# Performance work log

Measured on AMD Instinct MI355X. Metric: run time of the kernel, lower is better.

Reference implementation:

```python
import jax, jax.numpy as jnp
import numpy as np

B, S, E = 2, 2048, 1024
D_ATTN, H = 1024, 16
HD = D_ATTN // H
SCALE = 1.0 / np.sqrt(D_ATTN)
ROPE_BASE = 10000.0


def setup_inputs() -> dict:
    key = jax.random.key(0)
    ks = jax.random.split(key, 7)
    def w(k, shape, scale):
        return jax.random.normal(k, shape, dtype=jnp.float32) * scale
    return {
        "q": w(ks[0], (B, S, E), 1.0),
        "k": w(ks[1], (B, S, E), 1.0),
        "v": w(ks[2], (B, S, E), 1.0),
        "Wq": w(ks[3], (D_ATTN, E), E ** -0.5),
        "Wk": w(ks[4], (D_ATTN, E), E ** -0.5),
        "Wv": w(ks[5], (D_ATTN, E), E ** -0.5),
        "Wo": w(ks[6], (E, D_ATTN), D_ATTN ** -0.5),
    }


def _rope(x):
    # x: [B, H, S, HD]; interleaved-pair rotary embedding over the seq axis
    s, d = x.shape[2], x.shape[3]
    half = d // 2
    inv_freq = 1.0 / (ROPE_BASE ** (jnp.arange(half, dtype=jnp.float32) * 2.0 / d))
    ang = jnp.arange(s, dtype=jnp.float32)[:, None] * inv_freq[None, :]  # [S, half]
    cos, sin = jnp.cos(ang), jnp.sin(ang)
    xr = x.reshape(x.shape[:-1] + (half, 2))
    x0, x1 = xr[..., 0], xr[..., 1]
    o0 = x0 * cos - x1 * sin
    o1 = x0 * sin + x1 * cos
    return jnp.stack([o0, o1], axis=-1).reshape(x.shape)


def reference(q, k, v, Wq, Wk, Wv, Wo):
    # linear projections (nn.Linear with weight [out, in]): y = x @ W^T
    qh = (q @ Wq.T).reshape(B, S, H, HD).transpose(0, 2, 1, 3)  # [B,H,S,HD]
    kh = (k @ Wk.T).reshape(B, S, H, HD).transpose(0, 2, 1, 3)
    vh = (v @ Wv.T).reshape(B, S, H, HD).transpose(0, 2, 1, 3)
    qh = _rope(qh)
    kh = _rope(kh)
    # shifted-causal mask: disallow j >= i (diagonal masked), except (0,0) allowed
    i = jnp.arange(S)[:, None]
    j = jnp.arange(S)[None, :]
    masked = j >= i                              # triu incl. diagonal
    masked = masked.at[0, 0].set(False)          # keep (0,0) so row 0 isn't all -inf
    scores = jnp.einsum("bhsd,bhtd->bhst", qh, kh) * SCALE
    scores = jnp.where(masked, -jnp.inf, scores)
    probs = jax.nn.softmax(scores, axis=-1)      # dropout omitted (eval mode)
    ctx = jnp.einsum("bhst,bhtd->bhsd", probs, vh)
    ctx = ctx.transpose(0, 2, 1, 3).reshape(B, S, D_ATTN)
    return ctx @ Wo.T
```

## Files before the change

kernel.cpp:

```cpp
#include <hip/hip_runtime.h>
#include <hip/hip_bf16.h>

#define BATCH 2
#define SEQ   2048
#define EMB   1024
#define DATTN 1024
#define NH    16
#define HD    64
#define MM    (BATCH*SEQ)
#define SCALE 0.03125f
#define MINIT -1.0e30f
#define ROPE_COEF 0.41524101186f

using bf16x8 = __attribute__((ext_vector_type(8))) short;
using f32x4  = __attribute__((ext_vector_type(4))) float;

__device__ inline short f2bf(float x) {
    __hip_bfloat16 b = __float2bfloat16(x);
    return *reinterpret_cast<short*>(&b);
}

__device__ inline void gl_lds16(const short* g, short* l) {
    __builtin_amdgcn_global_load_lds(
        (const __attribute__((address_space(1))) unsigned int*)g,
        (__attribute__((address_space(3))) unsigned int*)l, 16, 0, 0);
}

__global__ __launch_bounds__(256)
void cvt_all(const float* __restrict__ q, const float* __restrict__ k,
             const float* __restrict__ v,
             const float* __restrict__ Wq, const float* __restrict__ Wk,
             const float* __restrict__ Wv, const float* __restrict__ Wo,
             short* __restrict__ dst)
{
    const long QKV = (long)MM * EMB;
    const long WSZ = (long)DATTN * EMB;
    const long i = ((long)blockIdx.x * 256 + threadIdx.x) * 4;
    const float* s;
    long off;
    if (i < 3 * QKV) {
        const int seg = (int)(i / QKV);
        off = i - (long)seg * QKV;
        s = (seg == 0) ? q : (seg == 1) ? k : v;
    } else {
        const long j = i - 3 * QKV;
        const int seg = (int)(j / WSZ);
        off = j - (long)seg * WSZ;
        s = (seg == 0) ? Wq : (seg == 1) ? Wk : (seg == 2) ? Wv : Wo;
    }
    float4 x = *(const float4*)(s + off);
    short4 y;
    y.x = f2bf(x.x); y.y = f2bf(x.y); y.z = f2bf(x.z); y.w = f2bf(x.w);
    *(short4*)(dst + i) = y;
}

__device__ inline void stage_tile(const short* g, short* lds, int wave, int lane) {
    #pragma unroll
    for (int qq = 0; qq < 2; ++qq) {
        const int r = wave * 32 + qq * 16 + (lane >> 2);
        gl_lds16(g + (long)r * EMB + (lane & 3) * 8, lds + (wave * 2 + qq) * 512);
    }
}

__global__ __launch_bounds__(256)
void gemm_proj_bf16(const short* __restrict__ qb, const short* __restrict__ kb,
                    const short* __restrict__ vb,
                    const short* __restrict__ wqb, const short* __restrict__ wkb,
                    const short* __restrict__ wvb,
                    short* __restrict__ Qb, short* __restrict__ Kb,
                    short* __restrict__ Vtb)
{
    const short* A; const short* B;
    if (blockIdx.z == 0)      { A = qb; B = wqb; }
    else if (blockIdx.z == 1) { A = kb; B = wkb; }
    else                      { A = vb; B = wvb; }

    __shared__ short sA[128 * 32];
    __shared__ short sB[128 * 32];

    const int tid  = threadIdx.x;
    const int wave = tid >> 6, lane = tid & 63;
    const int quad = lane >> 4, l16 = lane & 15;
    const int wm = (wave >> 1) * 64, wn = (wave & 1) * 64;
    const long m0 = (long)blockIdx.x * 128, n0 = (long)blockIdx.y * 128;

    f32x4 acc[4][4];
    #pragma unroll
    for (int i = 0; i < 4; ++i)
        #pragma unroll
        for (int j = 0; j < 4; ++j) acc[i][j] = (f32x4){0.f, 0.f, 0.f, 0.f};

    for (int kt = 0; kt < EMB; kt += 32) {
        __syncthreads();
        stage_tile(A + m0 * EMB + kt, sA, wave, lane);
        stage_tile(B + n0 * EMB + kt, sB, wave, lane);
        __syncthreads();

        bf16x8 af[4], bfr[4];
        #pragma unroll
        for (int rt = 0; rt < 4; ++rt)
            af[rt] = *(const bf16x8*)&sA[(wm + rt * 16 + l16) * 32 + quad * 8];
        #pragma unroll
        for (int ct = 0; ct < 4; ++ct)
            bfr[ct] = *(const bf16x8*)&sB[(wn + ct * 16 + l16) * 32 + quad * 8];
        #pragma unroll
        for (int rt = 0; rt < 4; ++rt)
            #pragma unroll
            for (int ct = 0; ct < 4; ++ct)
                acc[rt][ct] = __builtin_amdgcn_mfma_f32_16x16x32_bf16(
                    af[rt], bfr[ct], acc[rt][ct], 0, 0, 0);
    }

    if (blockIdx.z < 2) {
        short* C = (blockIdx.z == 0) ? Qb : Kb;
        const float scl = (blockIdx.z == 0) ? SCALE : 1.0f;
        const int odd = l16 & 1;
        #pragma unroll
        for (int ct = 0; ct < 4; ++ct) {
            const long col = n0 + wn + ct * 16 + l16;
            const int hh = (int)(col >> 6), dd = (int)(col & (HD - 1));
            const float invf = exp2f(-ROPE_COEF * (float)(dd >> 1));
            #pragma unroll
            for (int rt = 0; rt < 4; ++rt) {
                #pragma unroll
                for (int reg = 0; reg < 4; ++reg) {
                    const long row = m0 + wm + rt * 16 + quad * 4 + reg;
                    const int bb = (int)(row >> 11), ss = (int)(row & (SEQ - 1));
                    const float val = acc[rt][ct][reg];
                    const float prt = __shfl_xor(val, 1, 64);
                    float sn, cs;
                    __sincosf((float)ss * invf, &sn, &cs);
                    const float o = odd ? (prt * sn + val * cs)
                                        : (val * cs - prt * sn);
                    C[(((long)(bb * NH + hh)) << 17) + ((long)ss << 6) + dd] =
                        f2bf(o * scl);
                }
            }
        }
    } else {
        #pragma unroll
        for (int rt = 0; rt < 4; ++rt) {
            #pragma unroll
            for (int ct = 0; ct < 4; ++ct) {
                const long row0 = m0 + wm + rt * 16 + quad * 4;
                const long col  = n0 + wn + ct * 16 + l16;
                const int bb = (int)(row0 >> 11), ss = (int)(row0 & (SEQ - 1));
                const int hh = (int)(col >> 6),   dd = (int)(col & (HD - 1));
                short4 s4;
                s4.x = f2bf(acc[rt][ct][0]); s4.y = f2bf(acc[rt][ct][1]);
                s4.z = f2bf(acc[rt][ct][2]); s4.w = f2bf(acc[rt][ct][3]);
                *(short4*)&Vtb[(((long)(bb * NH + hh)) << 17) + ((long)dd << 11) + ss] = s4;
            }
        }
    }
}

__global__ __launch_bounds__(256)
void gemm_out_bf16(const short* __restrict__ Ab, const short* __restrict__ Bb,
                   float* __restrict__ C)
{
    __shared__ short sA[128 * 32];
    __shared__ short sB[128 * 32];

    const int tid  = threadIdx.x;
    const int wave = tid >> 6, lane = tid & 63;
    const int quad = lane >> 4, l16 = lane & 15;
    const int wm = (wave >> 1) * 64, wn = (wave & 1) * 64;
    const long m0 = (long)blockIdx.x * 128, n0 = (long)blockIdx.y * 128;

    f32x4 acc[4][4];
    #pragma unroll
    for (int i = 0; i < 4; ++i)
        #pragma unroll
        for (int j = 0; j < 4; ++j) acc[i][j] = (f32x4){0.f, 0.f, 0.f, 0.f};

    for (int kt = 0; kt < DATTN; kt += 32) {
        __syncthreads();
        stage_tile(Ab + m0 * DATTN + kt, sA, wave, lane);
        stage_tile(Bb + n0 * DATTN + kt, sB, wave, lane);
        __syncthreads();

        bf16x8 af[4], bfr[4];
        #pragma unroll
        for (int rt = 0; rt < 4; ++rt)
            af[rt] = *(const bf16x8*)&sA[(wm + rt * 16 + l16) * 32 + quad * 8];
        #pragma unroll
        for (int ct = 0; ct < 4; ++ct)
            bfr[ct] = *(const bf16x8*)&sB[(wn + ct * 16 + l16) * 32 + quad * 8];
        #pragma unroll
        for (int rt = 0; rt < 4; ++rt)
            #pragma unroll
            for (int ct = 0; ct < 4; ++ct)
                acc[rt][ct] = __builtin_amdgcn_mfma_f32_16x16x32_bf16(
                    af[rt], bfr[ct], acc[rt][ct], 0, 0, 0);
    }

    #pragma unroll
    for (int rt = 0; rt < 4; ++rt) {
        #pragma unroll
        for (int ct = 0; ct < 4; ++ct) {
            #pragma unroll
            for (int reg = 0; reg < 4; ++reg) {
                const long row = m0 + wm + rt * 16 + quad * 4 + reg;
                const long col = n0 + wn + ct * 16 + l16;
                C[row * EMB + col] = acc[rt][ct][reg];
            }
        }
    }
}

#define LDP 72

__global__ __launch_bounds__(256, 2)
void flash_attn_mfma(const short* __restrict__ Qb,
                     const short* __restrict__ Kb,
                     const short* __restrict__ Vtb,
                     short* __restrict__ ctx)
{
    const int id  = blockIdx.x;
    const int hi  = id >> 8;
    const int idx = id & 255;
    const int r   = idx & 7;
    const int s5  = idx >> 3;
    const int pi  = s5 & 3;
    const int ts8 = s5 >> 2;
    const int p   = r + 8 * pi;
    const int b   = p >> 4, h = p & 15;
    const int t   = hi ? ts8 : (15 - ts8);

    const int tid = threadIdx.x;
    const int wave = tid >> 6, lane = tid & 63;
    const int quad = lane >> 4, l16 = lane & 15;
    const int r0 = t * 128;

    __shared__ short sk2[2][64 * LDP];
    __shared__ short sv2[2][64 * LDP];
    __shared__ short sp[4][32 * LDP];

    const long base = ((long)(b * NH + h)) << 17;

    const int iq0 = r0 + wave * 32 + l16;
    const int iq1 = iq0 + 16;
    const int dtile = 2 * t + (wave >> 1);

    bf16x8 qf0[2], qf1[2];
    #pragma unroll
    for (int tt = 0; tt < 2; ++tt) {
        qf0[tt] = *(const bf16x8*)(Qb + base + (long)iq0 * HD + tt * 32 + quad * 8);
        qf1[tt] = *(const bf16x8*)(Qb + base + (long)iq1 * HD + tt * 32 + quad * 8);
    }

    f32x4 acc0[4], acc1[4];
    #pragma unroll
    for (int ct = 0; ct < 4; ++ct) {
        acc0[ct] = (f32x4){0.f, 0.f, 0.f, 0.f};
        acc1[ct] = (f32x4){0.f, 0.f, 0.f, 0.f};
    }
    float m0 = MINIT, l0 = 0.f;
    float m1 = MINIT, l1 = 0.f;

    const int njt = t + 1;

    #pragma unroll 1
    for (int jt = 0; jt < njt; ++jt) {
        const int jbase = jt * 128;

        __syncthreads();
        #pragma unroll
        for (int c = 0; c < 4; ++c) {
            int cc   = c * 256 + tid;
            int half = cc >> 9;
            int row  = (cc >> 3) & 63;
            int off  = (cc & 7) * 8;
            int4 tK = *(const int4*)(Kb + base
                + (long)(jbase + half * 64 + row) * HD + off);
            *(int4*)&sk2[half][row * LDP + off] = tK;
            int4 tV = *(const int4*)(Vtb + base
                + ((long)row << 11) + jbase + half * 64 + off);
            *(int4*)&sv2[half][row * LDP + off] = tV;
        }
        __syncthreads();

        #pragma unroll
        for (int half = 0; half < 2; ++half) {
            const int jt2 = 2 * jt + half;
            if (jt2 > dtile) continue;
            const int jb2 = jbase + half * 64;
            const short* skh = sk2[half];
            const short* svh = sv2[half];

            f32x4 s0[4], s1[4];
            #pragma unroll
            for (int ct = 0; ct < 4; ++ct) {
                bf16x8 k0 = *(const bf16x8*)&skh[(ct * 16 + l16) * LDP + quad * 8];
                bf16x8 k1 = *(const bf16x8*)&skh[(ct * 16 + l16) * LDP + 32 + quad * 8];
                f32x4 z0 = (f32x4){0.f, 0.f, 0.f, 0.f};
                z0 = __builtin_amdgcn_mfma_f32_16x16x32_bf16(k0, qf0[0], z0, 0, 0, 0);
                z0 = __builtin_amdgcn_mfma_f32_16x16x32_bf16(k1, qf0[1], z0, 0, 0, 0);
                s0[ct] = z0;
                f32x4 z1 = (f32x4){0.f, 0.f, 0.f, 0.f};
                z1 = __builtin_amdgcn_mfma_f32_16x16x32_bf16(k0, qf1[0], z1, 0, 0, 0);
                z1 = __builtin_amdgcn_mfma_f32_16x16x32_bf16(k1, qf1[1], z1, 0, 0, 0);
                s1[ct] = z1;
            }

            if (jt2 == dtile) {
                #pragma unroll
                for (int ct = 0; ct < 4; ++ct)
                    #pragma unroll
                    for (int rr = 0; rr < 4; ++rr) {
                        const int j = jb2 + ct * 16 + quad * 4 + rr;
                        if (!((j < iq0) || (iq0 == 0 && j == 0)))
                            s0[ct][rr] = -INFINITY;
                        if (!(j < iq1))
                            s1[ct][rr] = -INFINITY;
                    }
            }

            float mx0 = MINIT;
            #pragma unroll
            for (int ct = 0; ct < 4; ++ct)
                #pragma unroll
                for (int rr = 0; rr < 4; ++rr) mx0 = fmaxf(mx0, s0[ct][rr]);
            mx0 = fmaxf(mx0, __shfl_xor(mx0, 16, 64));
            mx0 = fmaxf(mx0, __shfl_xor(mx0, 32, 64));
            const float mn0 = fmaxf(m0, mx0);
            const float a0 = __expf(m0 - mn0);
            m0 = mn0;
            float ss0 = 0.f;
            #pragma unroll
            for (int ct = 0; ct < 4; ++ct)
                #pragma unroll
                for (int rr = 0; rr < 4; ++rr) {
                    const float e = __expf(s0[ct][rr] - mn0);
                    s0[ct][rr] = e;
                    ss0 += e;
                }
            ss0 += __shfl_xor(ss0, 16, 64);
            ss0 += __shfl_xor(ss0, 32, 64);
            l0 = l0 * a0 + ss0;

            float mx1 = MINIT;
            #pragma unroll
            for (int ct = 0; ct < 4; ++ct)
                #pragma unroll
                for (int rr = 0; rr < 4; ++rr) mx1 = fmaxf(mx1, s1[ct][rr]);
            mx1 = fmaxf(mx1, __shfl_xor(mx1, 16, 64));
            mx1 = fmaxf(mx1, __shfl_xor(mx1, 32, 64));
            const float mn1 = fmaxf(m1, mx1);
            const float a1 = __expf(m1 - mn1);
            m1 = mn1;
            float ss1 = 0.f;
            #pragma unroll
            for (int ct = 0; ct < 4; ++ct)
                #pragma unroll
                for (int rr = 0; rr < 4; ++rr) {
                    const float e = __expf(s1[ct][rr] - mn1);
                    s1[ct][rr] = e;
                    ss1 += e;
                }
            ss1 += __shfl_xor(ss1, 16, 64);
            ss1 += __shfl_xor(ss1, 32, 64);
            l1 = l1 * a1 + ss1;

            short* pw0 = sp[wave];
            short* pw1 = sp[wave] + 16 * LDP;
            #pragma unroll
            for (int ct = 0; ct < 4; ++ct) {
                short4 p4;
                p4.x = f2bf(s0[ct][0]); p4.y = f2bf(s0[ct][1]);
                p4.z = f2bf(s0[ct][2]); p4.w = f2bf(s0[ct][3]);
                *(short4*)&pw0[l16 * LDP + ct * 16 + quad * 4] = p4;
                short4 q4;
                q4.x = f2bf(s1[ct][0]); q4.y = f2bf(s1[ct][1]);
                q4.z = f2bf(s1[ct][2]); q4.w = f2bf(s1[ct][3]);
                *(short4*)&pw1[l16 * LDP + ct * 16 + quad * 4] = q4;
            }

            #pragma unroll
            for (int ct = 0; ct < 4; ++ct)
                #pragma unroll
                for (int rr = 0; rr < 4; ++rr) {
                    acc0[ct][rr] *= a0;
                    acc1[ct][rr] *= a1;
                }

            bf16x8 pf00 = *(const bf16x8*)&pw0[l16 * LDP + quad * 8];
            bf16x8 pf01 = *(const bf16x8*)&pw0[l16 * LDP + 32 + quad * 8];
            bf16x8 pf10 = *(const bf16x8*)&pw1[l16 * LDP + quad * 8];
            bf16x8 pf11 = *(const bf16x8*)&pw1[l16 * LDP + 32 + quad * 8];

            #pragma unroll
            for (int ct = 0; ct < 4; ++ct) {
                bf16x8 v0 = *(const bf16x8*)&svh[(ct * 16 + l16) * LDP + quad * 8];
                bf16x8 v1 = *(const bf16x8*)&svh[(ct * 16 + l16) * LDP + 32 + quad * 8];
                acc0[ct] = __builtin_amdgcn_mfma_f32_16x16x32_bf16(
                    v0, pf00, acc0[ct], 0, 0, 0);
                acc0[ct] = __builtin_amdgcn_mfma_f32_16x16x32_bf16(
                    v1, pf01, acc0[ct], 0, 0, 0);
                acc1[ct] = __builtin_amdgcn_mfma_f32_16x16x32_bf16(
                    v0, pf10, acc1[ct], 0, 0, 0);
                acc1[ct] = __builtin_amdgcn_mfma_f32_16x16x32_bf16(
                    v1, pf11, acc1[ct], 0, 0, 0);
            }
        }
    }

    {
        const float inv0 = 1.f / l0;
        short* orow = ctx + (long)(b * SEQ + iq0) * DATTN + h * HD;
        #pragma unroll
        for (int ct = 0; ct < 4; ++ct) {
            short4 o4;
            o4.x = f2bf(acc0[ct][0] * inv0);
            o4.y = f2bf(acc0[ct][1] * inv0);
            o4.z = f2bf(acc0[ct][2] * inv0);
            o4.w = f2bf(acc0[ct][3] * inv0);
            *(short4*)&orow[ct * 16 + quad * 4] = o4;
        }
    }
    {
        const float inv1 = 1.f / l1;
        short* orow = ctx + (long)(b * SEQ + iq1) * DATTN + h * HD;
        #pragma unroll
        for (int ct = 0; ct < 4; ++ct) {
            short4 o4;
            o4.x = f2bf(acc1[ct][0] * inv1);
            o4.y = f2bf(acc1[ct][1] * inv1);
            o4.z = f2bf(acc1[ct][2] * inv1);
            o4.w = f2bf(acc1[ct][3] * inv1);
            *(short4*)&orow[ct * 16 + quad * 4] = o4;
        }
    }
}

extern "C" void kernel_launch(void* const* d_in, const int* in_sizes, int n_in,
                              void* d_out, int out_size, void* d_ws, size_t ws_size,
                              hipStream_t stream) {
    const float* q  = (const float*)d_in[0];
    const float* k  = (const float*)d_in[1];
    const float* v  = (const float*)d_in[2];
    const float* Wq = (const float*)d_in[3];
    const float* Wk = (const float*)d_in[4];
    const float* Wv = (const float*)d_in[5];
    const float* Wo = (const float*)d_in[6];
    float* out = (float*)d_out;

    const long QKV = (long)MM * EMB;
    const long WSZ = (long)DATTN * EMB;
    short* basep = (short*)d_ws;
    short* qb  = basep;
    short* kb  = qb + QKV;
    short* vb  = kb + QKV;
    short* wqb = vb + QKV;
    short* wkb = wqb + WSZ;
    short* wvb = wkb + WSZ;
    short* wob = wvb + WSZ;
    short* Qb  = wob + WSZ;
    short* Kb  = Qb + QKV;
    short* Vtb = Kb + QKV;
    short* ctx = Vtb + QKV;

    cvt_all<<<16384, 256, 0, stream>>>(q, k, v, Wq, Wk, Wv, Wo, qb);

    gemm_proj_bf16<<<dim3(MM / 128, DATTN / 128, 3), 256, 0, stream>>>(
        qb, kb, vb, wqb, wkb, wvb, Qb, Kb, Vtb);

    flash_attn_mfma<<<512, 256, 0, stream>>>(Qb, Kb, Vtb, ctx);

    gemm_out_bf16<<<dim3(MM / 128, EMB / 128), 256, 0, stream>>>(ctx, wob, out);
}
```

Baseline: 230.0 us.

## Use direct global-to-LDS loads with XOR swizzle in attention; narrow output GEMM tile

```diff
diff --git a/kernel.cpp b/kernel.cpp
--- a/kernel.cpp
+++ b/kernel.cpp
@@ -160,37 +160,39 @@
                    float* __restrict__ C)
 {
     __shared__ short sA[128 * 32];
-    __shared__ short sB[128 * 32];
+    __shared__ short sB[64 * 32];
 
     const int tid  = threadIdx.x;
     const int wave = tid >> 6, lane = tid & 63;
     const int quad = lane >> 4, l16 = lane & 15;
-    const int wm = (wave >> 1) * 64, wn = (wave & 1) * 64;
-    const long m0 = (long)blockIdx.x * 128, n0 = (long)blockIdx.y * 128;
-
-    f32x4 acc[4][4];
+    const int wm = (wave >> 1) * 64, wn = (wave & 1) * 32;
+    const long m0 = (long)blockIdx.x * 128, n0 = (long)blockIdx.y * 64;
+
+    f32x4 acc[4][2];
     #pragma unroll
     for (int i = 0; i < 4; ++i)
         #pragma unroll
-        for (int j = 0; j < 4; ++j) acc[i][j] = (f32x4){0.f, 0.f, 0.f, 0.f};
+        for (int j = 0; j < 2; ++j) acc[i][j] = (f32x4){0.f, 0.f, 0.f, 0.f};
 
     for (int kt = 0; kt < DATTN; kt += 32) {
         __syncthreads();
         stage_tile(Ab + m0 * DATTN + kt, sA, wave, lane);
-        stage_tile(Bb + n0 * DATTN + kt, sB, wave, lane);
-        __syncthreads();
-
-        bf16x8 af[4], bfr[4];
+        gl_lds16(Bb + n0 * DATTN + kt
+                     + (long)(wave * 16 + (lane >> 2)) * DATTN + (lane & 3) * 8,
+                 sB + wave * 512);
+        __syncthreads();
+
+        bf16x8 af[4], bfr[2];
         #pragma unroll
         for (int rt = 0; rt < 4; ++rt)
             af[rt] = *(const bf16x8*)&sA[(wm + rt * 16 + l16) * 32 + quad * 8];
         #pragma unroll
-        for (int ct = 0; ct < 4; ++ct)
+        for (int ct = 0; ct < 2; ++ct)
             bfr[ct] = *(const bf16x8*)&sB[(wn + ct * 16 + l16) * 32 + quad * 8];
         #pragma unroll
         for (int rt = 0; rt < 4; ++rt)
             #pragma unroll
-            for (int ct = 0; ct < 4; ++ct)
+            for (int ct = 0; ct < 2; ++ct)
                 acc[rt][ct] = __builtin_amdgcn_mfma_f32_16x16x32_bf16(
                     af[rt], bfr[ct], acc[rt][ct], 0, 0, 0);
     }
@@ -198,7 +200,7 @@
     #pragma unroll
     for (int rt = 0; rt < 4; ++rt) {
         #pragma unroll
-        for (int ct = 0; ct < 4; ++ct) {
+        for (int ct = 0; ct < 2; ++ct) {
             #pragma unroll
             for (int reg = 0; reg < 4; ++reg) {
                 const long row = m0 + wm + rt * 16 + quad * 4 + reg;
@@ -209,7 +211,8 @@
     }
 }
 
-#define LDP 72
+#define KLD 64
+#define PLD 72
 
 __global__ __launch_bounds__(256, 2)
 void flash_attn_mfma(const short* __restrict__ Qb,
@@ -233,15 +236,16 @@
     const int quad = lane >> 4, l16 = lane & 15;
     const int r0 = t * 128;
 
-    __shared__ short sk2[2][64 * LDP];
-    __shared__ short sv2[2][64 * LDP];
-    __shared__ short sp[4][32 * LDP];
+    __shared__ short sk[2 * 64 * KLD];
+    __shared__ short sv[2 * 64 * KLD];
+    __shared__ short sp[4][32 * PLD];
 
     const long base = ((long)(b * NH + h)) << 17;
 
     const int iq0 = r0 + wave * 32 + l16;
     const int iq1 = iq0 + 16;
     const int dtile = 2 * t + (wave >> 1);
+    const int rsw = l16 & 7;
 
     bf16x8 qf0[2], qf1[2];
     #pragma unroll
@@ -268,16 +272,14 @@
         __syncthreads();
         #pragma unroll
         for (int c = 0; c < 4; ++c) {
-            int cc   = c * 256 + tid;
-            int half = cc >> 9;
-            int row  = (cc >> 3) & 63;
-            int off  = (cc & 7) * 8;
-            int4 tK = *(const int4*)(Kb + base
-                + (long)(jbase + half * 64 + row) * HD + off);
-            *(int4*)&sk2[half][row * LDP + off] = tK;
-            int4 tV = *(const int4*)(Vtb + base
-                + ((long)row << 11) + jbase + half * 64 + off);
-            *(int4*)&sv2[half][row * LDP + off] = tV;
+            const int cc   = c * 256 + tid;
+            const int half = cc >> 9;
+            const int row  = (cc >> 3) & 63;
+            const int sch  = (cc & 7) ^ (row & 7);
+            gl_lds16(Kb + base + (long)(jbase + half * 64 + row) * HD + sch * 8,
+                     sk + ((c * 256 + wave * 64) << 3));
+            gl_lds16(Vtb + base + ((long)row << 11) + jbase + half * 64 + sch * 8,
+                     sv + ((c * 256 + wave * 64) << 3));
         }
         __syncthreads();
 
@@ -286,14 +288,16 @@
             const int jt2 = 2 * jt + half;
             if (jt2 > dtile) continue;
             const int jb2 = jbase + half * 64;
-            const short* skh = sk2[half];
-            const short* svh = sv2[half];
+            const short* skh = sk + half * 64 * KLD;
+            const short* svh = sv + half * 64 * KLD;
 
             f32x4 s0[4], s1[4];
+            __builtin_amdgcn_s_setprio(1);
             #pragma unroll
             for (int ct = 0; ct < 4; ++ct) {
-                bf16x8 k0 = *(const bf16x8*)&skh[(ct * 16 + l16) * LDP + quad * 8];
-                bf16x8 k1 = *(const bf16x8*)&skh[(ct * 16 + l16) * LDP + 32 + quad * 8];
+                const int rr16 = (ct * 16 + l16) * KLD;
+                bf16x8 k0 = *(const bf16x8*)&skh[rr16 + ((quad ^ rsw) << 3)];
+                bf16x8 k1 = *(const bf16x8*)&skh[rr16 + (((4 + quad) ^ rsw) << 3)];
                 f32x4 z0 = (f32x4){0.f, 0.f, 0.f, 0.f};
                 z0 = __builtin_amdgcn_mfma_f32_16x16x32_bf16(k0, qf0[0], z0, 0, 0, 0);
                 z0 = __builtin_amdgcn_mfma_f32_16x16x32_bf16(k1, qf0[1], z0, 0, 0, 0);
@@ -303,6 +307,7 @@
                 z1 = __builtin_amdgcn_mfma_f32_16x16x32_bf16(k1, qf1[1], z1, 0, 0, 0);
                 s1[ct] = z1;
             }
+            __builtin_amdgcn_s_setprio(0);
 
             if (jt2 == dtile) {
                 #pragma unroll
@@ -364,17 +369,17 @@
             l1 = l1 * a1 + ss1;
 
             short* pw0 = sp[wave];
-            short* pw1 = sp[wave] + 16 * LDP;
+            short* pw1 = sp[wave] + 16 * PLD;
             #pragma unroll
             for (int ct = 0; ct < 4; ++ct) {
                 short4 p4;
                 p4.x = f2bf(s0[ct][0]); p4.y = f2bf(s0[ct][1]);
                 p4.z = f2bf(s0[ct][2]); p4.w = f2bf(s0[ct][3]);
-                *(short4*)&pw0[l16 * LDP + ct * 16 + quad * 4] = p4;
+                *(short4*)&pw0[l16 * PLD + ct * 16 + quad * 4] = p4;
                 short4 q4;
                 q4.x = f2bf(s1[ct][0]); q4.y = f2bf(s1[ct][1]);
                 q4.z = f2bf(s1[ct][2]); q4.w = f2bf(s1[ct][3]);
-                *(short4*)&pw1[l16 * LDP + ct * 16 + quad * 4] = q4;
+                *(short4*)&pw1[l16 * PLD + ct * 16 + quad * 4] = q4;
             }
 
             #pragma unroll
@@ -385,15 +390,17 @@
                     acc1[ct][rr] *= a1;
                 }
 
-            bf16x8 pf00 = *(const bf16x8*)&pw0[l16 * LDP + quad * 8];
-            bf16x8 pf01 = *(const bf16x8*)&pw0[l16 * LDP + 32 + quad * 8];
-            bf16x8 pf10 = *(const bf16x8*)&pw1[l16 * LDP + quad * 8];
-            bf16x8 pf11 = *(const bf16x8*)&pw1[l16 * LDP + 32 + quad * 8];
-
+            bf16x8 pf00 = *(const bf16x8*)&pw0[l16 * PLD + quad * 8];
+            bf16x8 pf01 = *(const bf16x8*)&pw0[l16 * PLD + 32 + quad * 8];
+            bf16x8 pf10 = *(const bf16x8*)&pw1[l16 * PLD + quad * 8];
+            bf16x8 pf11 = *(const bf16x8*)&pw1[l16 * PLD + 32 + quad * 8];
+
+            __builtin_amdgcn_s_setprio(1);
             #pragma unroll
             for (int ct = 0; ct < 4; ++ct) {
-                bf16x8 v0 = *(const bf16x8*)&svh[(ct * 16 + l16) * LDP + quad * 8];
-                bf16x8 v1 = *(const bf16x8*)&svh[(ct * 16 + l16) * LDP + 32 + quad * 8];
+                const int rr16 = (ct * 16 + l16) * KLD;
+                bf16x8 v0 = *(const bf16x8*)&svh[rr16 + ((quad ^ rsw) << 3)];
+                bf16x8 v1 = *(const bf16x8*)&svh[rr16 + (((4 + quad) ^ rsw) << 3)];
                 acc0[ct] = __builtin_amdgcn_mfma_f32_16x16x32_bf16(
                     v0, pf00, acc0[ct], 0, 0, 0);
                 acc0[ct] = __builtin_amdgcn_mfma_f32_16x16x32_bf16(
@@ -403,6 +410,7 @@
                 acc1[ct] = __builtin_amdgcn_mfma_f32_16x16x32_bf16(
                     v1, pf11, acc1[ct], 0, 0, 0);
             }
+            __builtin_amdgcn_s_setprio(0);
         }
     }
 
@@ -468,5 +476,5 @@
 
     flash_attn_mfma<<<512, 256, 0, stream>>>(Qb, Kb, Vtb, ctx);
 
-    gemm_out_bf16<<<dim3(MM / 128, EMB / 128), 256, 0, stream>>>(ctx, wob, out);
-}
+    gemm_out_bf16<<<dim3(MM / 128, EMB / 64), 256, 0, stream>>>(ctx, wob, out);
+}
```

New measurement: 222.4 us. 1.03x faster.
